# Optimization experiments

Hardware: AMD Instinct MI355X
Metric: run time of the kernel (lower is better)

## Reference

```python
import jax, jax.numpy as jnp
import numpy as np

N_NODES = 50000
N_EDGES = 800000
D = 64


def setup_inputs() -> dict:
    key = jax.random.key(0)
    ks = jax.random.split(key, 8)
    x = jax.random.normal(ks[0], (N_NODES, D), dtype=jnp.float32)
    src = jax.random.randint(ks[1], (N_EDGES,), 0, N_NODES, dtype=jnp.int32)
    dst = jax.random.randint(ks[2], (N_EDGES,), 0, N_NODES, dtype=jnp.int32)
    s = 1.0 / np.sqrt(D)
    w1_0 = jax.random.uniform(ks[3], (D, D), jnp.float32, -s, s)
    w2_0 = jax.random.uniform(ks[4], (D, D), jnp.float32, -s, s)
    w1_1 = jax.random.uniform(ks[5], (D, D), jnp.float32, -s, s)
    w2_1 = jax.random.uniform(ks[6], (D, D), jnp.float32, -s, s)
    b = jnp.zeros((D,), jnp.float32)
    return {"x": x, "src": src, "dst": dst,
            "w1_0": w1_0, "b1_0": b, "w2_0": w2_0, "b2_0": b,
            "w1_1": w1_1, "b1_1": b, "w2_1": w2_1, "b2_1": b}


def _gin_layer(x, src, dst, w1, b1, w2, b2):
    # sum aggregation over edges: agg[i] = sum_{(j->i) in E} x[j]
    agg = jax.ops.segment_sum(x[src], dst, num_segments=N_NODES)
    h = x + agg  # (1 + eps) * x + agg, eps = 0 (DGL GINConv default)
    h = jnp.tanh(h @ w1 + b1)
    return h @ w2 + b2


def reference(x, src, dst, w1_0, b1_0, w2_0, b2_0, w1_1, b1_1, w2_1, b2_1):
    x = _gin_layer(x, src, dst, w1_0, b1_0, w2_0, b2_0)
    x = _gin_layer(x, src, dst, w1_1, b1_1, w2_1, b2_1)
    return x
```

## Files before the change

kernel.cpp:

```cpp
#include <hip/hip_runtime.h>

#define D 64
#define CAP 56

typedef __attribute__((ext_vector_type(8))) short short8;
typedef __attribute__((ext_vector_type(4))) float f32x4;

__device__ __forceinline__ unsigned short f2bf(float f) {
    unsigned u = __float_as_uint(f);
    u = (u + 0x7fff + ((u >> 16) & 1)) >> 16;
    return (unsigned short)u;
}
__device__ __forceinline__ float bf_lo(unsigned u) { return __uint_as_float(u << 16); }
__device__ __forceinline__ float bf_hi(unsigned u) { return __uint_as_float(u & 0xffff0000u); }

__global__ __launch_bounds__(256) void convert_kernel(
    const float* __restrict__ x, unsigned short* __restrict__ xb, int n4)
{
    int i = blockIdx.x * blockDim.x + threadIdx.x;
    if (i >= n4) return;
    float4 v = *(const float4*)(x + i * 4);
    ushort4 o;
    o.x = f2bf(v.x); o.y = f2bf(v.y); o.z = f2bf(v.z); o.w = f2bf(v.w);
    *(ushort4*)(xb + i * 4) = o;
}

__global__ __launch_bounds__(256) void prep_weights_kernel(
    const float* __restrict__ w1_0, const float* __restrict__ w2_0,
    const float* __restrict__ w1_1, const float* __restrict__ w2_1,
    unsigned short* __restrict__ wt)
{
    int i = blockIdx.x * blockDim.x + threadIdx.x;
    int m = i >> 12, r = i & 4095;
    int n = r >> 6, k = r & 63;
    const float* w = (m == 0) ? w1_0 : (m == 1) ? w2_0 : (m == 2) ? w1_1 : w2_1;
    wt[i] = f2bf(w[k * 64 + n]);
}

__global__ __launch_bounds__(256) void scatter_kernel(
    const int* __restrict__ src, const int* __restrict__ dst,
    int* __restrict__ deg, unsigned short* __restrict__ buf, int n_edges)
{
    int e = blockIdx.x * blockDim.x + threadIdx.x;
    if (e >= n_edges) return;
    int d = dst[e];
    int p = atomicAdd(&deg[d], 1);
    if (p < CAP) buf[(size_t)d * CAP + p] = (unsigned short)src[e];
}

__global__ __launch_bounds__(256) void gather_kernel(
    const unsigned short* __restrict__ xb, const int* __restrict__ deg,
    const unsigned short* __restrict__ buf, unsigned short* __restrict__ aggb)
{
    const int tid  = threadIdx.x;
    const int lane = tid & 63;
    const int wave = tid >> 6;
    const int n    = blockIdx.x * 4 + wave;

    const int slot = lane >> 3;
    const int fc   = (lane & 7) << 3;

    int dd = deg[n];
    dd = dd < CAP ? dd : CAP;

    int my_idx = buf[(size_t)n * CAP + (lane < CAP ? lane : CAP - 1)];

    float a[8] = {0.f, 0.f, 0.f, 0.f, 0.f, 0.f, 0.f, 0.f};
    if (slot == 0) {
        uint4 u = *(const uint4*)(xb + (size_t)n * D + fc);
        a[0] = bf_lo(u.x); a[1] = bf_hi(u.x);
        a[2] = bf_lo(u.y); a[3] = bf_hi(u.y);
        a[4] = bf_lo(u.z); a[5] = bf_hi(u.z);
        a[6] = bf_lo(u.w); a[7] = bf_hi(u.w);
    }

    int iters = (dd + 7) >> 3;
    #pragma unroll 2
    for (int g = 0; g < iters; ++g) {
        int jj = (g << 3) + slot;
        int s  = __shfl(my_idx, jj);
        uint4 v = *(const uint4*)(xb + (size_t)s * D + fc);
        float m = (jj < dd) ? 1.0f : 0.0f;
        a[0] += bf_lo(v.x) * m; a[1] += bf_hi(v.x) * m;
        a[2] += bf_lo(v.y) * m; a[3] += bf_hi(v.y) * m;
        a[4] += bf_lo(v.z) * m; a[5] += bf_hi(v.z) * m;
        a[6] += bf_lo(v.w) * m; a[7] += bf_hi(v.w) * m;
    }

    #pragma unroll
    for (int m = 8; m <= 32; m <<= 1) {
        #pragma unroll
        for (int q = 0; q < 8; ++q) a[q] += __shfl_xor(a[q], m);
    }
    if (slot == 0) {
        uint4 o;
        o.x = (unsigned)f2bf(a[0]) | ((unsigned)f2bf(a[1]) << 16);
        o.y = (unsigned)f2bf(a[2]) | ((unsigned)f2bf(a[3]) << 16);
        o.z = (unsigned)f2bf(a[4]) | ((unsigned)f2bf(a[5]) << 16);
        o.w = (unsigned)f2bf(a[6]) | ((unsigned)f2bf(a[7]) << 16);
        *(uint4*)(aggb + (size_t)n * D + fc) = o;
    }
}

template <bool WRITE_BF16>
__global__ __launch_bounds__(256) void gin_dense_mfma(
    const unsigned short* __restrict__ hb, int n_nodes,
    const unsigned short* __restrict__ w1t, const float* __restrict__ b1,
    const unsigned short* __restrict__ w2t, const float* __restrict__ b2,
    float* __restrict__ out_f, unsigned short* __restrict__ out_b)
{
    __shared__ unsigned short sh [64][72];
    __shared__ unsigned short st [64][72];
    __shared__ unsigned short sw1[64][72];
    __shared__ unsigned short sw2[64][72];

    const int t    = threadIdx.x;
    const int lane = t & 63;
    const int wave = t >> 6;
    const int quad = lane >> 4;
    const int col  = lane & 15;
    const int nb   = blockIdx.x * 64;

    for (int c = t; c < 512; c += 256) {
        int row = c >> 3, c8 = (c & 7) << 3;
        *(uint4*)&sh [row][c8] = *(const uint4*)(hb  + (size_t)(nb + row) * D + c8);
        *(uint4*)&sw1[row][c8] = *(const uint4*)(w1t + row * D + c8);
        *(uint4*)&sw2[row][c8] = *(const uint4*)(w2t + row * D + c8);
    }
    __syncthreads();

    const int arow = 16 * wave + col;
    const int koff = quad << 3;

    short8 a0 = *(const short8*)&sh[arow][koff];
    short8 a1 = *(const short8*)&sh[arow][32 + koff];

    #pragma unroll
    for (int nt = 0; nt < 4; ++nt) {
        int n = (nt << 4) + col;
        short8 bw0 = *(const short8*)&sw1[n][koff];
        short8 bw1 = *(const short8*)&sw1[n][32 + koff];
        float bv = b1[n];
        f32x4 c = {bv, bv, bv, bv};
        c = __builtin_amdgcn_mfma_f32_16x16x32_bf16(a0, bw0, c, 0, 0, 0);
        c = __builtin_amdgcn_mfma_f32_16x16x32_bf16(a1, bw1, c, 0, 0, 0);
        #pragma unroll
        for (int r = 0; r < 4; ++r)
            st[16 * wave + (quad << 2) + r][n] = f2bf(tanhf(c[r]));
    }

    short8 p0 = *(const short8*)&st[arow][koff];
    short8 p1 = *(const short8*)&st[arow][32 + koff];

    #pragma unroll
    for (int nt = 0; nt < 4; ++nt) {
        int n = (nt << 4) + col;
        short8 bw0 = *(const short8*)&sw2[n][koff];
        short8 bw1 = *(const short8*)&sw2[n][32 + koff];
        float bv = b2[n];
        f32x4 c = {bv, bv, bv, bv};
        c = __builtin_amdgcn_mfma_f32_16x16x32_bf16(p0, bw0, c, 0, 0, 0);
        c = __builtin_amdgcn_mfma_f32_16x16x32_bf16(p1, bw1, c, 0, 0, 0);
        #pragma unroll
        for (int r = 0; r < 4; ++r) {
            int row = nb + 16 * wave + (quad << 2) + r;
            if (WRITE_BF16) {
                out_b[(size_t)row * D + n] = f2bf(c[r]);
            } else if (row < n_nodes) {
                out_f[(size_t)row * D + n] = c[r];
            }
        }
    }
}

extern "C" void kernel_launch(void* const* d_in, const int* in_sizes, int n_in,
                              void* d_out, int out_size, void* d_ws, size_t ws_size,
                              hipStream_t stream)
{
    const float* x    = (const float*)d_in[0];
    const int*   src  = (const int*)  d_in[1];
    const int*   dst  = (const int*)  d_in[2];
    const float* w1_0 = (const float*)d_in[3];
    const float* b1_0 = (const float*)d_in[4];
    const float* w2_0 = (const float*)d_in[5];
    const float* b2_0 = (const float*)d_in[6];
    const float* w1_1 = (const float*)d_in[7];
    const float* b1_1 = (const float*)d_in[8];
    const float* w2_1 = (const float*)d_in[9];
    const float* b2_1 = (const float*)d_in[10];
    float* out = (float*)d_out;

    const int n_nodes = in_sizes[0] / D;
    const int n_edges = in_sizes[1];
    const int n_pad   = (n_nodes + 63) & ~63;

    int*            deg  = (int*)d_ws;
    unsigned short* buf  = (unsigned short*)(deg + n_nodes);
    unsigned short* aggb = buf  + (size_t)n_nodes * CAP;
    unsigned short* xb   = aggb + (size_t)n_pad * D;
    unsigned short* x1b  = xb   + (size_t)n_pad * D;
    unsigned short* wt   = x1b  + (size_t)n_pad * D;

    hipMemsetAsync(deg, 0, (size_t)n_nodes * sizeof(int) + (size_t)n_nodes * CAP * sizeof(unsigned short), stream);
    convert_kernel<<<(n_nodes * D / 4 + 255) / 256, 256, 0, stream>>>(x, xb, n_nodes * D / 4);
    prep_weights_kernel<<<64, 256, 0, stream>>>(w1_0, w2_0, w1_1, w2_1, wt);
    scatter_kernel<<<(n_edges + 255) / 256, 256, 0, stream>>>(src, dst, deg, buf, n_edges);

    const int gather_blocks = n_nodes / 4;
    const int dense_blocks  = n_pad / 64;

    gather_kernel<<<gather_blocks, 256, 0, stream>>>(xb, deg, buf, aggb);
    gin_dense_mfma<true><<<dense_blocks, 256, 0, stream>>>(
        aggb, n_nodes, wt, b1_0, wt + 4096, b2_0, nullptr, x1b);
    gather_kernel<<<gather_blocks, 256, 0, stream>>>(x1b, deg, buf, aggb);
    gin_dense_mfma<false><<<dense_blocks, 256, 0, stream>>>(
        aggb, n_nodes, wt + 8192, b1_1, wt + 12288, b2_1, out, nullptr);
}
```

Baseline: 191.2 us.

## Merge prep kernels into one launch and fully unroll gather loads

Three preprocessing kernels (scatter, convert, weight prep) become a single launch with block-range dispatch, which removes launch gaps and lets the independent work overlap. The gather kernel now always issues all 7 neighbour loads up front with masking, instead of a dynamic loop over the actual degree. This raises memory-level parallelism, at the cost of extra loads for low-degree nodes (they hit valid row indices, so they are masked but still fetched) and more registers.

```diff
diff --git a/kernel.cpp b/kernel.cpp
--- a/kernel.cpp
+++ b/kernel.cpp
@@ -14,38 +14,37 @@
 __device__ __forceinline__ float bf_lo(unsigned u) { return __uint_as_float(u << 16); }
 __device__ __forceinline__ float bf_hi(unsigned u) { return __uint_as_float(u & 0xffff0000u); }
 
-__global__ __launch_bounds__(256) void convert_kernel(
-    const float* __restrict__ x, unsigned short* __restrict__ xb, int n4)
-{
-    int i = blockIdx.x * blockDim.x + threadIdx.x;
-    if (i >= n4) return;
-    float4 v = *(const float4*)(x + i * 4);
-    ushort4 o;
-    o.x = f2bf(v.x); o.y = f2bf(v.y); o.z = f2bf(v.z); o.w = f2bf(v.w);
-    *(ushort4*)(xb + i * 4) = o;
-}
-
-__global__ __launch_bounds__(256) void prep_weights_kernel(
+__global__ __launch_bounds__(256) void prep_scatter_kernel(
+    const int* __restrict__ src, const int* __restrict__ dst,
+    int* __restrict__ deg, unsigned short* __restrict__ buf, int n_edges, int nsb,
+    const float* __restrict__ x, unsigned short* __restrict__ xb, int n4, int ncb,
     const float* __restrict__ w1_0, const float* __restrict__ w2_0,
     const float* __restrict__ w1_1, const float* __restrict__ w2_1,
     unsigned short* __restrict__ wt)
 {
-    int i = blockIdx.x * blockDim.x + threadIdx.x;
-    int m = i >> 12, r = i & 4095;
-    int n = r >> 6, k = r & 63;
-    const float* w = (m == 0) ? w1_0 : (m == 1) ? w2_0 : (m == 2) ? w1_1 : w2_1;
-    wt[i] = f2bf(w[k * 64 + n]);
-}
-
-__global__ __launch_bounds__(256) void scatter_kernel(
-    const int* __restrict__ src, const int* __restrict__ dst,
-    int* __restrict__ deg, unsigned short* __restrict__ buf, int n_edges)
-{
-    int e = blockIdx.x * blockDim.x + threadIdx.x;
-    if (e >= n_edges) return;
-    int d = dst[e];
-    int p = atomicAdd(&deg[d], 1);
-    if (p < CAP) buf[(size_t)d * CAP + p] = (unsigned short)src[e];
+    const int b = blockIdx.x;
+    if (b < nsb) {
+        int e = b * 256 + threadIdx.x;
+        if (e < n_edges) {
+            int d = dst[e];
+            int p = atomicAdd(&deg[d], 1);
+            if (p < CAP) buf[(size_t)d * CAP + p] = (unsigned short)src[e];
+        }
+    } else if (b < nsb + ncb) {
+        int i = (b - nsb) * 256 + threadIdx.x;
+        if (i < n4) {
+            float4 v = *(const float4*)(x + i * 4);
+            ushort4 o;
+            o.x = f2bf(v.x); o.y = f2bf(v.y); o.z = f2bf(v.z); o.w = f2bf(v.w);
+            *(ushort4*)(xb + i * 4) = o;
+        }
+    } else {
+        int i = (b - nsb - ncb) * 256 + threadIdx.x;
+        int m = i >> 12, r = i & 4095;
+        int n = r >> 6, k = r & 63;
+        const float* w = (m == 0) ? w1_0 : (m == 1) ? w2_0 : (m == 2) ? w1_1 : w2_1;
+        wt[i] = f2bf(w[k * 64 + n]);
+    }
 }
 
 __global__ __launch_bounds__(256) void gather_kernel(
@@ -60,32 +59,35 @@
     const int slot = lane >> 3;
     const int fc   = (lane & 7) << 3;
 
+    int my_idx = buf[(size_t)n * CAP + (lane < CAP ? lane : CAP - 1)];
     int dd = deg[n];
     dd = dd < CAP ? dd : CAP;
 
-    int my_idx = buf[(size_t)n * CAP + (lane < CAP ? lane : CAP - 1)];
+    uint4 u = make_uint4(0u, 0u, 0u, 0u);
+    if (slot == 0) u = *(const uint4*)(xb + (size_t)n * D + fc);
+
+    int s[7];
+    #pragma unroll
+    for (int g = 0; g < 7; ++g) s[g] = __shfl(my_idx, (g << 3) + slot);
+
+    uint4 v[7];
+    #pragma unroll
+    for (int g = 0; g < 7; ++g)
+        v[g] = *(const uint4*)(xb + (size_t)s[g] * D + fc);
 
     float a[8] = {0.f, 0.f, 0.f, 0.f, 0.f, 0.f, 0.f, 0.f};
-    if (slot == 0) {
-        uint4 u = *(const uint4*)(xb + (size_t)n * D + fc);
-        a[0] = bf_lo(u.x); a[1] = bf_hi(u.x);
-        a[2] = bf_lo(u.y); a[3] = bf_hi(u.y);
-        a[4] = bf_lo(u.z); a[5] = bf_hi(u.z);
-        a[6] = bf_lo(u.w); a[7] = bf_hi(u.w);
-    }
-
-    int iters = (dd + 7) >> 3;
-    #pragma unroll 2
-    for (int g = 0; g < iters; ++g) {
-        int jj = (g << 3) + slot;
-        int s  = __shfl(my_idx, jj);
-        uint4 v = *(const uint4*)(xb + (size_t)s * D + fc);
-        float m = (jj < dd) ? 1.0f : 0.0f;
-        a[0] += bf_lo(v.x) * m; a[1] += bf_hi(v.x) * m;
-        a[2] += bf_lo(v.y) * m; a[3] += bf_hi(v.y) * m;
-        a[4] += bf_lo(v.z) * m; a[5] += bf_hi(v.z) * m;
-        a[6] += bf_lo(v.w) * m; a[7] += bf_hi(v.w) * m;
-    }
+    #pragma unroll
+    for (int g = 0; g < 7; ++g) {
+        float m = ((g << 3) + slot) < dd ? 1.0f : 0.0f;
+        a[0] += bf_lo(v[g].x) * m; a[1] += bf_hi(v[g].x) * m;
+        a[2] += bf_lo(v[g].y) * m; a[3] += bf_hi(v[g].y) * m;
+        a[4] += bf_lo(v[g].z) * m; a[5] += bf_hi(v[g].z) * m;
+        a[6] += bf_lo(v[g].w) * m; a[7] += bf_hi(v[g].w) * m;
+    }
+    a[0] += bf_lo(u.x); a[1] += bf_hi(u.x);
+    a[2] += bf_lo(u.y); a[3] += bf_hi(u.y);
+    a[4] += bf_lo(u.z); a[5] += bf_hi(u.z);
+    a[6] += bf_lo(u.w); a[7] += bf_hi(u.w);
 
     #pragma unroll
     for (int m = 8; m <= 32; m <<= 1) {
@@ -201,10 +203,15 @@
     unsigned short* x1b  = xb   + (size_t)n_pad * D;
     unsigned short* wt   = x1b  + (size_t)n_pad * D;
 
+    const int n4  = n_nodes * D / 4;
+    const int nsb = (n_edges + 255) / 256;
+    const int ncb = (n4 + 255) / 256;
+
     hipMemsetAsync(deg, 0, (size_t)n_nodes * sizeof(int) + (size_t)n_nodes * CAP * sizeof(unsigned short), stream);
-    convert_kernel<<<(n_nodes * D / 4 + 255) / 256, 256, 0, stream>>>(x, xb, n_nodes * D / 4);
-    prep_weights_kernel<<<64, 256, 0, stream>>>(w1_0, w2_0, w1_1, w2_1, wt);
-    scatter_kernel<<<(n_edges + 255) / 256, 256, 0, stream>>>(src, dst, deg, buf, n_edges);
+    prep_scatter_kernel<<<nsb + ncb + 64, 256, 0, stream>>>(
+        src, dst, deg, buf, n_edges, nsb,
+        x, xb, n4, ncb,
+        w1_0, w2_0, w1_1, w2_1, wt);
 
     const int gather_blocks = n_nodes / 4;
     const int dense_blocks  = n_pad / 64;
```

After: 189.9 us. No clear change (-0.7%).
